# Kernel tuning notes

Measured on AMD Instinct MI355X. Metric: run time of the kernel, lower is better.

## Reference

```python
import jax, jax.numpy as jnp
import numpy as np

N = 100000      # nodes
E = 1600000     # edges
F_IN = 512      # num_node_features
HID = 128       # hidden_dim (GCN2Conv channels)
C = 64          # num_classes
L = 8           # n_layers
ALPHA = 0.1
THETA = 0.5


def setup_inputs() -> dict:
    key = jax.random.key(0)
    ks = jax.random.split(key, 7)
    x = jax.random.normal(ks[0], (N, F_IN), jnp.float32)
    edge_index = jax.random.randint(ks[1], (2, E), 0, N, dtype=jnp.int64)
    # fcs[0]: Linear(F_IN, HID); stored as [in, out] so forward is x @ w + b
    w_in = jax.random.normal(ks[2], (F_IN, HID), jnp.float32) / np.sqrt(F_IN)
    b_in = jnp.zeros((HID,), jnp.float32)
    # one shared [H, H] weight per GCN2Conv layer (shared_weights=True)
    conv_w = jax.random.normal(ks[3], (L, HID, HID), jnp.float32) / np.sqrt(HID)
    # fcs[-1]: Linear(HID, C)
    w_out = jax.random.normal(ks[4], (HID, C), jnp.float32) / np.sqrt(HID)
    b_out = jnp.zeros((C,), jnp.float32)
    return dict(x=x, edge_index=edge_index, w_in=w_in, b_in=b_in,
                conv_w=conv_w, w_out=w_out, b_out=b_out)


def _gcn_norm(edge_index, num_nodes):
    # PyG gcn_norm with add_self_loops=True, edge_weight=1
    loops = jnp.arange(num_nodes, dtype=edge_index.dtype)
    src = jnp.concatenate([edge_index[0], loops])
    dst = jnp.concatenate([edge_index[1], loops])
    deg = jax.ops.segment_sum(jnp.ones_like(dst, jnp.float32), dst,
                              num_segments=num_nodes)
    dinv = jnp.where(deg > 0, jax.lax.rsqrt(jnp.maximum(deg, 1e-12)), 0.0)
    norm = dinv[src] * dinv[dst]  # [E + N]
    return src, dst, norm


def reference(x, edge_index, w_in, b_in, conv_w, w_out, b_out):
    src, dst, norm = _gcn_norm(edge_index, N)
    h = x @ w_in + b_in          # fcs[0]; [N, HID]
    h0 = h                       # initial residual
    for l in range(L):
        beta = float(np.log(THETA / (l + 1) + 1.0))
        # sparse neighbor aggregation: out[i] = sum_e norm[e] * h[src[e]]
        agg = jax.ops.segment_sum(h[src] * norm[:, None], dst, num_segments=N)
        s = (1.0 - ALPHA) * agg + ALPHA * h0           # initial residual mix
        h = jax.nn.elu((1.0 - beta) * s + beta * (s @ conv_w[l]))  # identity mapping
        # dropout omitted (eval mode / training=False)
    logits = h @ w_out + b_out   # fcs[-1]
    return jax.nn.log_softmax(logits, axis=-1)
```

## Files before the change

### kernel.cpp

```cpp
#include <hip/hip_runtime.h>
#include <math.h>

#define N_NODES 100000
#define N_EDGES 1600000
#define F_IN    512
#define HID     128
#define NCLS    64
#define NLAYERS 8
#define NT      (N_NODES / 16)
#define NSCANB  ((N_NODES + 255) / 256)

typedef __attribute__((ext_vector_type(8))) short short8;
typedef __attribute__((ext_vector_type(4))) float float4v;

#define SWZB(b) ((b) ^ ((((b) >> 8) & 3) << 4))
#define SWZC(b) ((b) ^ ((((b) >> 8) & 7) << 4))

__device__ inline unsigned short f2bf(float f) {
    unsigned int u = __float_as_uint(f);
    unsigned int r = u + 0x7fffu + ((u >> 16) & 1u);
    return (unsigned short)(r >> 16);
}
__device__ inline float bf2f(unsigned short h) {
    return __uint_as_float(((unsigned int)h) << 16);
}
__device__ inline uint4 pack8(const unsigned short* v) {
    uint4 u;
    u.x = (unsigned)v[0] | ((unsigned)v[1] << 16);
    u.y = (unsigned)v[2] | ((unsigned)v[3] << 16);
    u.z = (unsigned)v[4] | ((unsigned)v[5] << 16);
    u.w = (unsigned)v[6] | ((unsigned)v[7] << 16);
    return u;
}
__device__ inline void bf8_fma(float* a, uint4 u, float v) {
    a[0] += v * __uint_as_float(u.x << 16);
    a[1] += v * __uint_as_float(u.x & 0xffff0000u);
    a[2] += v * __uint_as_float(u.y << 16);
    a[3] += v * __uint_as_float(u.y & 0xffff0000u);
    a[4] += v * __uint_as_float(u.z << 16);
    a[5] += v * __uint_as_float(u.z & 0xffff0000u);
    a[6] += v * __uint_as_float(u.w << 16);
    a[7] += v * __uint_as_float(u.w & 0xffff0000u);
}
__device__ inline void unpack8(float* f, uint4 u) {
    f[0] = __uint_as_float(u.x << 16); f[1] = __uint_as_float(u.x & 0xffff0000u);
    f[2] = __uint_as_float(u.y << 16); f[3] = __uint_as_float(u.y & 0xffff0000u);
    f[4] = __uint_as_float(u.z << 16); f[5] = __uint_as_float(u.z & 0xffff0000u);
    f[6] = __uint_as_float(u.w << 16); f[7] = __uint_as_float(u.w & 0xffff0000u);
}
__device__ inline void split_into(short8& ahi, short8& alo, int j, float f) {
    unsigned short h = f2bf(f);
    ahi[j] = (short)h;
    alo[j] = (short)f2bf(f - bf2f(h));
}


__global__ __launch_bounds__(256) void cnt_init(int* __restrict__ cnt) {
    int i = blockIdx.x * 256 + threadIdx.x;
    if (i < N_NODES) cnt[i] = 0;
}
__global__ __launch_bounds__(256) void cnt_count(const int* __restrict__ dst,
                                                 int* __restrict__ cnt) {
    int e = blockIdx.x * 256 + threadIdx.x;
    if (e < N_EDGES) atomicAdd(&cnt[dst[e]], 1);
}
__global__ __launch_bounds__(256) void make_dinv(const int* __restrict__ cnt,
                                                 float* __restrict__ dinv) {
    int i = blockIdx.x * 256 + threadIdx.x;
    if (i < N_NODES) dinv[i] = rsqrtf((float)(cnt[i] + 1));
}
__global__ __launch_bounds__(256) void scan_block(const int* __restrict__ cnt,
                                                  int* __restrict__ partial,
                                                  int* __restrict__ bsum) {
    __shared__ int tmp[256];
    int t = threadIdx.x, i = blockIdx.x * 256 + t;
    int v = (i < N_NODES) ? cnt[i] : 0;
    tmp[t] = v;
    __syncthreads();
#pragma unroll
    for (int off = 1; off < 256; off <<= 1) {
        int add = (t >= off) ? tmp[t - off] : 0;
        __syncthreads();
        tmp[t] += add;
        __syncthreads();
    }
    if (i < N_NODES) partial[i] = tmp[t];
    if (t == 255) bsum[blockIdx.x] = tmp[255];
}
__global__ __launch_bounds__(256) void scan_b2(int* __restrict__ b) {
    __shared__ int ps[256];
    int t = threadIdx.x;
    int i0 = 2 * t, i1 = 2 * t + 1;
    int v0 = (i0 < NSCANB) ? b[i0] : 0;
    int v1 = (i1 < NSCANB) ? b[i1] : 0;
    int s = v0 + v1;
    ps[t] = s;
    __syncthreads();
#pragma unroll
    for (int off = 1; off < 256; off <<= 1) {
        int add = (t >= off) ? ps[t - off] : 0;
        __syncthreads();
        ps[t] += add;
        __syncthreads();
    }
    int excl = ps[t] - s;
    if (i0 < NSCANB) b[i0] = excl;
    if (i1 < NSCANB) b[i1] = excl + v0;
}
__global__ __launch_bounds__(256) void finalize_rowptr(const int* __restrict__ cnt,
                                                       const int* __restrict__ partial,
                                                       const int* __restrict__ bsum,
                                                       int* __restrict__ row_ptr,
                                                       int* __restrict__ cursor) {
    int i = blockIdx.x * 256 + threadIdx.x;
    if (i < N_NODES) {
        int ex = partial[i] - cnt[i] + bsum[blockIdx.x];
        row_ptr[i] = ex;
        cursor[i]  = ex;
        if (i == N_NODES - 1) row_ptr[N_NODES] = ex + cnt[i];
    }
}
__global__ __launch_bounds__(256) void scatter_edges(const int* __restrict__ srcI,
                                                     const int* __restrict__ dstI,
                                                     const float* __restrict__ dinv,
                                                     int* __restrict__ cursor,
                                                     int2* __restrict__ rec) {
    int e = blockIdx.x * 256 + threadIdx.x;
    if (e < N_EDGES) {
        int s = srcI[e], d = dstI[e];
        int pos = atomicAdd(&cursor[d], 1);
        rec[pos] = make_int2(s, __float_as_int(dinv[s] * dinv[d]));
    }
}

__global__ __launch_bounds__(64) void conv_win(const float* __restrict__ w,
                                               unsigned short* __restrict__ wip) {
    int nt = blockIdx.x >> 4;
    int c  = blockIdx.x & 15;
    int lane = threadIdx.x;
    int n  = nt * 16 + (lane & 15);
    int kb = c * 32 + (lane >> 4) * 8;
    unsigned short hi[8], lo[8];
#pragma unroll
    for (int j = 0; j < 8; j++) {
        float v = w[(size_t)(kb + j) * HID + n];
        hi[j] = f2bf(v);
        lo[j] = f2bf(v - bf2f(hi[j]));
    }
    size_t base = ((size_t)c * 8 + nt) * 1024 + (size_t)lane * 8;
    *(uint4*)&wip[base]       = pack8(hi);
    *(uint4*)&wip[base + 512] = pack8(lo);
}

__global__ __launch_bounds__(64) void conv_wl(const float* __restrict__ cw,
                                              unsigned short* __restrict__ wlp) {
    int l  = blockIdx.x >> 5;
    int nt = (blockIdx.x >> 2) & 7;
    int c  = blockIdx.x & 3;
    int lane = threadIdx.x;
    float beta = logf(0.5f / (float)(l + 1) + 1.0f);
    int n  = nt * 16 + (lane & 15);
    int kb = c * 32 + (lane >> 4) * 8;
    const float* W = cw + (size_t)l * HID * HID;
    unsigned short hi[8], lo[8];
#pragma unroll
    for (int j = 0; j < 8; j++) {
        int k = kb + j;
        float v = beta * W[(size_t)k * HID + n] + ((k == n) ? (1.0f - beta) : 0.0f);
        hi[j] = f2bf(v);
        lo[j] = f2bf(v - bf2f(hi[j]));
    }
    size_t base = (size_t)l * 32768 + ((size_t)c * 8 + nt) * 1024 + (size_t)lane * 8;
    *(uint4*)&wlp[base]       = pack8(hi);
    *(uint4*)&wlp[base + 512] = pack8(lo);
}

__global__ __launch_bounds__(64) void conv_wout(const float* __restrict__ w,
                                                unsigned short* __restrict__ wop) {
    int nt = blockIdx.x >> 2;
    int c  = blockIdx.x & 3;
    int lane = threadIdx.x;
    int n  = nt * 16 + (lane & 15);
    int kb = c * 32 + (lane >> 4) * 8;
    unsigned short hi[8], lo[8];
#pragma unroll
    for (int j = 0; j < 8; j++) {
        float v = w[(size_t)(kb + j) * NCLS + n];
        hi[j] = f2bf(v);
        lo[j] = f2bf(v - bf2f(hi[j]));
    }
    size_t base = ((size_t)nt * 4 + c) * 1024 + (size_t)lane * 8;
    *(uint4*)&wop[base]       = pack8(hi);
    *(uint4*)&wop[base + 512] = pack8(lo);
}

__global__ __launch_bounds__(256) void in_gemm_mfma(const float* __restrict__ x,
        const unsigned short* __restrict__ wip, const float* __restrict__ bias,
        unsigned short* __restrict__ hb, unsigned short* __restrict__ h0b) {
    __shared__ unsigned short wlds[8192];
    __shared__ unsigned short tile[64][136];
    int tid = threadIdx.x;
    int wave = tid >> 6, lane = tid & 63;
    int t = blockIdx.x * 4 + wave;
    int m = lane & 15, q = lane >> 4;
    int tc = (t < NT) ? t : (NT - 1);

    const uint4* wg = (const uint4*)wip;
    uint4 pf0 = wg[tid];
    uint4 pf1 = wg[tid + 256];
    uint4 pf2 = wg[tid + 512];
    uint4 pf3 = wg[tid + 768];

    float4v acc[8];
#pragma unroll
    for (int nt = 0; nt < 8; nt++) acc[nt] = (float4v){0.f, 0.f, 0.f, 0.f};
    const float* xr = x + (size_t)(tc * 16 + m) * F_IN + q * 8;
    uint4* wl4 = (uint4*)wlds;

    for (int c = 0; c < 16; c++) {
        wl4[tid] = pf0; wl4[tid + 256] = pf1; wl4[tid + 512] = pf2; wl4[tid + 768] = pf3;
        __syncthreads();
        if (c < 15) {
            const uint4* wn = wg + (size_t)(c + 1) * 1024;
            pf0 = wn[tid]; pf1 = wn[tid + 256]; pf2 = wn[tid + 512]; pf3 = wn[tid + 768];
        }
        float4 x0 = *(const float4*)(xr + c * 32);
        float4 x1 = *(const float4*)(xr + c * 32 + 4);
        short8 ahi, alo;
        split_into(ahi, alo, 0, x0.x); split_into(ahi, alo, 1, x0.y);
        split_into(ahi, alo, 2, x0.z); split_into(ahi, alo, 3, x0.w);
        split_into(ahi, alo, 4, x1.x); split_into(ahi, alo, 5, x1.y);
        split_into(ahi, alo, 6, x1.z); split_into(ahi, alo, 7, x1.w);
#pragma unroll
        for (int nt = 0; nt < 8; nt++) {
            short8 bhi = *(short8*)&wlds[nt * 1024 + lane * 8];
            short8 blo = *(short8*)&wlds[nt * 1024 + 512 + lane * 8];
            acc[nt] = __builtin_amdgcn_mfma_f32_16x16x32_bf16(ahi, bhi, acc[nt], 0, 0, 0);
            acc[nt] = __builtin_amdgcn_mfma_f32_16x16x32_bf16(ahi, blo, acc[nt], 0, 0, 0);
            acc[nt] = __builtin_amdgcn_mfma_f32_16x16x32_bf16(alo, bhi, acc[nt], 0, 0, 0);
        }
        __syncthreads();
    }

    if (t < NT) {
#pragma unroll
        for (int nt = 0; nt < 8; nt++) {
            float bb = bias[nt * 16 + m];
#pragma unroll
            for (int r = 0; r < 4; r++)
                tile[wave * 16 + q * 4 + r][nt * 16 + m] = f2bf(acc[nt][r] + bb);
        }
    }
    __syncthreads();

    int nl = tid >> 2, part = tid & 3;
    int node = blockIdx.x * 64 + nl;
    if (node < N_NODES) {
        uint4* d1 = (uint4*)&hb [(size_t)node * HID + part * 32];
        uint4* d2 = (uint4*)&h0b[(size_t)node * HID + part * 32];
#pragma unroll
        for (int j = 0; j < 4; j++) {
            uint4 u = *(uint4*)&tile[nl][part * 32 + j * 8];
            d1[j] = u; d2[j] = u;
        }
    }
}

template <int LAST>
__global__ __launch_bounds__(256, 4) void spmm_gemm(const int* __restrict__ row_ptr,
        const int2* __restrict__ rec, const float* __restrict__ dinv,
        const unsigned short* __restrict__ hin, const unsigned short* __restrict__ h0b,
        const unsigned short* __restrict__ wlp, const unsigned short* __restrict__ wop,
        const float* __restrict__ obias, void* __restrict__ outp) {
    __shared__ __align__(16) unsigned short afr[16384];
    int tid = threadIdx.x;
    int wave = tid >> 6, lane = tid & 63;
    int qu = lane >> 4, fl = lane & 15;
    char* af = (char*)afr;

    int base = blockIdx.x * 64 + wave * 16;
#pragma unroll 1
    for (int g = 0; g < 4; ++g) {
        int node = base + g * 4 + qu;
        int nc = (node < N_NODES) ? node : (N_NODES - 1);
        int e0 = row_ptr[nc], e1 = row_ptr[nc + 1];
        float dd = dinv[nc];
        uint4 hv = *(const uint4*)(hin + (size_t)nc * HID + fl * 8);
        uint4 zv = *(const uint4*)(h0b + (size_t)nc * HID + fl * 8);
        float a[8] = {0.f, 0.f, 0.f, 0.f, 0.f, 0.f, 0.f, 0.f};
        int e = e0;
        for (; e + 7 < e1; e += 8) {
            int2 r0 = rec[e],     r1 = rec[e + 1], r2 = rec[e + 2], r3 = rec[e + 3];
            int2 r4 = rec[e + 4], r5 = rec[e + 5], r6 = rec[e + 6], r7 = rec[e + 7];
            uint4 u0 = *(const uint4*)(hin + (size_t)r0.x * HID + fl * 8);
            uint4 u1 = *(const uint4*)(hin + (size_t)r1.x * HID + fl * 8);
            uint4 u2 = *(const uint4*)(hin + (size_t)r2.x * HID + fl * 8);
            uint4 u3 = *(const uint4*)(hin + (size_t)r3.x * HID + fl * 8);
            uint4 u4 = *(const uint4*)(hin + (size_t)r4.x * HID + fl * 8);
            uint4 u5 = *(const uint4*)(hin + (size_t)r5.x * HID + fl * 8);
            uint4 u6 = *(const uint4*)(hin + (size_t)r6.x * HID + fl * 8);
            uint4 u7 = *(const uint4*)(hin + (size_t)r7.x * HID + fl * 8);
            bf8_fma(a, u0, __int_as_float(r0.y));
            bf8_fma(a, u1, __int_as_float(r1.y));
            bf8_fma(a, u2, __int_as_float(r2.y));
            bf8_fma(a, u3, __int_as_float(r3.y));
            bf8_fma(a, u4, __int_as_float(r4.y));
            bf8_fma(a, u5, __int_as_float(r5.y));
            bf8_fma(a, u6, __int_as_float(r6.y));
            bf8_fma(a, u7, __int_as_float(r7.y));
        }
        for (; e + 3 < e1; e += 4) {
            int2 r0 = rec[e], r1 = rec[e + 1], r2 = rec[e + 2], r3 = rec[e + 3];
            uint4 u0 = *(const uint4*)(hin + (size_t)r0.x * HID + fl * 8);
            uint4 u1 = *(const uint4*)(hin + (size_t)r1.x * HID + fl * 8);
            uint4 u2 = *(const uint4*)(hin + (size_t)r2.x * HID + fl * 8);
            uint4 u3 = *(const uint4*)(hin + (size_t)r3.x * HID + fl * 8);
            bf8_fma(a, u0, __int_as_float(r0.y));
            bf8_fma(a, u1, __int_as_float(r1.y));
            bf8_fma(a, u2, __int_as_float(r2.y));
            bf8_fma(a, u3, __int_as_float(r3.y));
        }
        for (; e < e1; ++e) {
            int2 r0 = rec[e];
            uint4 u0 = *(const uint4*)(hin + (size_t)r0.x * HID + fl * 8);
            bf8_fma(a, u0, __int_as_float(r0.y));
        }
        float d2 = dd * dd;
        float hvf[8], zvf[8];
        unpack8(hvf, hv);
        unpack8(zvf, zv);
        short8 ohi, olo;
#pragma unroll
        for (int j = 0; j < 8; ++j) {
            float o = 0.9f * (a[j] + d2 * hvf[j]) + 0.1f * zvf[j];
            split_into(ohi, olo, j, o);
        }
        int mrow = g * 4 + qu;
        int b0 = wave * 8192 + (fl >> 2) * 2048 + (fl & 3) * 256 + mrow * 16;
        *(short8*)(af + SWZB(b0)) = ohi;
        *(short8*)(af + SWZB(b0 + 1024)) = olo;
    }
    __syncthreads();

    float4v acc[8];
#pragma unroll
    for (int nt = 0; nt < 8; ++nt) acc[nt] = (float4v){0.f, 0.f, 0.f, 0.f};
    const short8* wp8 = (const short8*)wlp;
#pragma unroll
    for (int c = 0; c < 4; ++c) {
        int rb = wave * 8192 + c * 2048 + lane * 16;
        short8 ahi = *(const short8*)(af + SWZB(rb));
        short8 alo = *(const short8*)(af + SWZB(rb + 1024));
#pragma unroll
        for (int nt = 0; nt < 8; ++nt) {
            short8 bhi = wp8[(size_t)(c * 8 + nt) * 128 + lane];
            short8 blo = wp8[(size_t)(c * 8 + nt) * 128 + 64 + lane];
            acc[nt] = __builtin_amdgcn_mfma_f32_16x16x32_bf16(ahi, bhi, acc[nt], 0, 0, 0);
            acc[nt] = __builtin_amdgcn_mfma_f32_16x16x32_bf16(ahi, blo, acc[nt], 0, 0, 0);
            acc[nt] = __builtin_amdgcn_mfma_f32_16x16x32_bf16(alo, bhi, acc[nt], 0, 0, 0);
        }
    }

    if (LAST) {
        int t = blockIdx.x * 4 + wave;
        __syncthreads();
        char* wb = af + wave * 8192;
        if (t < NT) {
#pragma unroll
            for (int nt = 0; nt < 8; ++nt) {
#pragma unroll
                for (int r = 0; r < 4; ++r) {
                    float v = acc[nt][r];
                    v = (v > 0.f) ? v : (expf(v) - 1.0f);
                    unsigned short h = f2bf(v);
                    unsigned short l = f2bf(v - bf2f(h));
                    int b = (qu * 4 + r) * 256 + (nt * 16 + fl) * 2;
                    *(unsigned short*)(wb + SWZC(b)) = h;
                    *(unsigned short*)(wb + 4096 + SWZC(b)) = l;
                }
            }
        }
        __syncthreads();
        if (t < NT) {
            float4v oc[4];
#pragma unroll
            for (int nt = 0; nt < 4; ++nt) oc[nt] = (float4v){0.f, 0.f, 0.f, 0.f};
            const short8* wq = (const short8*)wop;
#pragma unroll
            for (int c = 0; c < 4; ++c) {
                int rb = fl * 256 + (c * 32 + qu * 8) * 2;
                short8 ahi = *(const short8*)(wb + SWZC(rb));
                short8 alo = *(const short8*)(wb + 4096 + SWZC(rb));
#pragma unroll
                for (int nt = 0; nt < 4; ++nt) {
                    short8 bhi = wq[(size_t)(nt * 4 + c) * 128 + lane];
                    short8 blo = wq[(size_t)(nt * 4 + c) * 128 + 64 + lane];
                    oc[nt] = __builtin_amdgcn_mfma_f32_16x16x32_bf16(ahi, bhi, oc[nt], 0, 0, 0);
                    oc[nt] = __builtin_amdgcn_mfma_f32_16x16x32_bf16(ahi, blo, oc[nt], 0, 0, 0);
                    oc[nt] = __builtin_amdgcn_mfma_f32_16x16x32_bf16(alo, bhi, oc[nt], 0, 0, 0);
                }
            }
            float* out = (float*)outp;
            float bn[4];
#pragma unroll
            for (int nt = 0; nt < 4; ++nt) bn[nt] = obias[nt * 16 + fl];
#pragma unroll
            for (int r = 0; r < 4; ++r) {
                float v0 = oc[0][r] + bn[0], v1 = oc[1][r] + bn[1];
                float v2 = oc[2][r] + bn[2], v3 = oc[3][r] + bn[3];
                float mx = fmaxf(fmaxf(v0, v1), fmaxf(v2, v3));
#pragma unroll
                for (int msk = 1; msk < 16; msk <<= 1) mx = fmaxf(mx, __shfl_xor(mx, msk));
                float ssum = expf(v0 - mx) + expf(v1 - mx) + expf(v2 - mx) + expf(v3 - mx);
#pragma unroll
                for (int msk = 1; msk < 16; msk <<= 1) ssum += __shfl_xor(ssum, msk);
                float lg = mx + logf(ssum);
                size_t ob = (size_t)(t * 16 + qu * 4 + r) * NCLS + fl;
                out[ob]      = v0 - lg;
                out[ob + 16] = v1 - lg;
                out[ob + 32] = v2 - lg;
                out[ob + 48] = v3 - lg;
            }
        }
    } else {
        __syncthreads();
        unsigned short (*tile)[136] = (unsigned short (*)[136])afr;
#pragma unroll
        for (int nt = 0; nt < 8; ++nt) {
#pragma unroll
            for (int r = 0; r < 4; ++r) {
                float v = acc[nt][r];
                v = (v > 0.f) ? v : (expf(v) - 1.0f);
                tile[wave * 16 + qu * 4 + r][nt * 16 + fl] = f2bf(v);
            }
        }
        __syncthreads();
        unsigned short* hout = (unsigned short*)outp;
        int nl = tid >> 2, part = tid & 3;
        int node = blockIdx.x * 64 + nl;
        if (node < N_NODES) {
            uint4* d1 = (uint4*)&hout[(size_t)node * HID + part * 32];
#pragma unroll
            for (int j = 0; j < 4; ++j) d1[j] = *(uint4*)&tile[nl][part * 32 + j * 8];
        }
    }
}


extern "C" void kernel_launch(void* const* d_in, const int* in_sizes, int n_in,
                              void* d_out, int out_size, void* d_ws, size_t ws_size,
                              hipStream_t stream) {
    const float* x      = (const float*)d_in[0];
    const int*   ei     = (const int*)  d_in[1];
    const float* w_in   = (const float*)d_in[2];
    const float* b_in   = (const float*)d_in[3];
    const float* conv_w = (const float*)d_in[4];
    const float* w_out  = (const float*)d_in[5];
    const float* b_out  = (const float*)d_in[6];
    float* out = (float*)d_out;

    const int* srcI = ei;
    const int* dstI = ei + N_EDGES;

    char* ws = (char*)d_ws;
    float* dinv    = (float*)(ws + 0x000000);
    int*   cnt     = (int*)  (ws + 0x080000);
    int*   partial = (int*)  (ws + 0x100000);
    int*   bsum    = (int*)  (ws + 0x180000);
    int*   row_ptr = (int*)  (ws + 0x190000);
    int*   cursor  = (int*)  (ws + 0x200000);
    int2*  rec     = (int2*) (ws + 0x280000);
    unsigned short* wip = (unsigned short*)(ws + 0xF00000);
    unsigned short* wlp = (unsigned short*)(ws + 0xF40000);
    unsigned short* wop = (unsigned short*)(ws + 0xFC0000);
    unsigned short* hb  = (unsigned short*)(ws + 0x1000000);
    unsigned short* h0b = hb + (size_t)N_NODES * HID;
    unsigned short* hb2 = h0b + (size_t)N_NODES * HID;

    int gN = (N_NODES + 255) / 256;
    int gE = (N_EDGES + 255) / 256;
    int gT = (NT + 3) / 4;

    cnt_init<<<gN, 256, 0, stream>>>(cnt);
    cnt_count<<<gE, 256, 0, stream>>>(dstI, cnt);
    make_dinv<<<gN, 256, 0, stream>>>(cnt, dinv);
    scan_block<<<NSCANB, 256, 0, stream>>>(cnt, partial, bsum);
    scan_b2<<<1, 256, 0, stream>>>(bsum);
    finalize_rowptr<<<NSCANB, 256, 0, stream>>>(cnt, partial, bsum, row_ptr, cursor);
    scatter_edges<<<gE, 256, 0, stream>>>(srcI, dstI, dinv, cursor, rec);

    conv_win<<<128, 64, 0, stream>>>(w_in, wip);
    conv_wl<<<256, 64, 0, stream>>>(conv_w, wlp);
    conv_wout<<<16, 64, 0, stream>>>(w_out, wop);

    in_gemm_mfma<<<gT, 256, 0, stream>>>(x, wip, b_in, hb, h0b);

    unsigned short* cur = hb;
    unsigned short* nxt = hb2;
    for (int l = 0; l < NLAYERS; l++) {
        const unsigned short* wl = wlp + (size_t)l * 32768;
        if (l < NLAYERS - 1) {
            spmm_gemm<0><<<gT, 256, 0, stream>>>(row_ptr, rec, dinv, cur, h0b, wl,
                                                 nullptr, nullptr, nxt);
            unsigned short* t = cur; cur = nxt; nxt = t;
        } else {
            spmm_gemm<1><<<gT, 256, 0, stream>>>(row_ptr, rec, dinv, cur, h0b, wl,
                                                 wop, b_out, out);
        }
    }
}
```

Measured before the change: 1.189 ms.

## Split SpMM from GEMM using feature-sliced planes for cache-resident gathers

Node features are stored as 8 feature planes of 16 channels each, and the fused SpMM+GEMM kernel is split in two. A new spmm_slice kernel aggregates one plane at a time, with block index interleaving slices, so each gather touches a 3.2MB plane that can stay in cache. It writes fp32 mixed features to an intermediate buffer, and a separate gemm_layer kernel reads them back for the MFMA transform. This trades an extra fp32 round trip through memory and an extra launch per layer for better gather locality, and it re-reads the edge records once per slice.

After: 2.140 ms. 80.0% more time.

```diff
diff --git a/kernel.cpp b/kernel.cpp
--- a/kernel.cpp
+++ b/kernel.cpp
@@ -9,6 +9,9 @@
 #define NLAYERS 8
 #define NT      (N_NODES / 16)
 #define NSCANB  ((N_NODES + 255) / 256)
+#define PLANEH  ((size_t)N_NODES * 16)
+#define PLANES  ((size_t)N_NODES * 16)
+#define GSLICE  (((N_NODES + 127) / 128) * 8)
 
 typedef __attribute__((ext_vector_type(8))) short short8;
 typedef __attribute__((ext_vector_type(4))) float float4v;
@@ -196,7 +199,7 @@
 
 __global__ __launch_bounds__(256) void in_gemm_mfma(const float* __restrict__ x,
         const unsigned short* __restrict__ wip, const float* __restrict__ bias,
-        unsigned short* __restrict__ hb, unsigned short* __restrict__ h0b) {
+        unsigned short* __restrict__ h_sm, unsigned short* __restrict__ h0_sm) {
     __shared__ unsigned short wlds[8192];
     __shared__ unsigned short tile[64][136];
     int tid = threadIdx.x;
@@ -253,23 +256,99 @@
     }
     __syncthreads();
 
-    int nl = tid >> 2, part = tid & 3;
-    int node = blockIdx.x * 64 + nl;
-    if (node < N_NODES) {
-        uint4* d1 = (uint4*)&hb [(size_t)node * HID + part * 32];
-        uint4* d2 = (uint4*)&h0b[(size_t)node * HID + part * 32];
-#pragma unroll
-        for (int j = 0; j < 4; j++) {
-            uint4 u = *(uint4*)&tile[nl][part * 32 + j * 8];
-            d1[j] = u; d2[j] = u;
-        }
-    }
+#pragma unroll
+    for (int k = 0; k < 2; k++) {
+        int c2 = tid + k * 256;
+        int plane = c2 >> 6, nl = c2 & 63;
+        int node = blockIdx.x * 64 + nl;
+        if (node < N_NODES) {
+            uint4 u0 = *(uint4*)&tile[nl][plane * 16];
+            uint4 u1 = *(uint4*)&tile[nl][plane * 16 + 8];
+            size_t off = (size_t)plane * PLANEH + (size_t)node * 16;
+            *(uint4*)&h_sm[off]      = u0; *(uint4*)&h_sm[off + 8]  = u1;
+            *(uint4*)&h0_sm[off]     = u0; *(uint4*)&h0_sm[off + 8] = u1;
+        }
+    }
+}
+
+__global__ __launch_bounds__(256) void spmm_slice(const int* __restrict__ row_ptr,
+        const int2* __restrict__ rec, const float* __restrict__ dinv,
+        const unsigned short* __restrict__ h_sm, const unsigned short* __restrict__ h0_sm,
+        float* __restrict__ s_sm) {
+    int slice = blockIdx.x & 7;
+    int tile  = blockIdx.x >> 3;
+    int node  = tile * 128 + (threadIdx.x >> 1);
+    int half  = threadIdx.x & 1;
+    if (node >= N_NODES) return;
+    const unsigned short* hp = h_sm + (size_t)slice * PLANEH;
+    int e0 = row_ptr[node], e1 = row_ptr[node + 1];
+    float dd = dinv[node];
+    uint4 hv = *(const uint4*)(hp + (size_t)node * 16 + half * 8);
+    uint4 zv = *(const uint4*)(h0_sm + (size_t)slice * PLANEH + (size_t)node * 16 + half * 8);
+    float a[8] = {0.f, 0.f, 0.f, 0.f, 0.f, 0.f, 0.f, 0.f};
+    const long long* rl = (const long long*)rec;
+    int e = e0;
+    for (; e + 7 < e1; e += 8) {
+        long long q0 = __builtin_nontemporal_load(rl + e);
+        long long q1 = __builtin_nontemporal_load(rl + e + 1);
+        long long q2 = __builtin_nontemporal_load(rl + e + 2);
+        long long q3 = __builtin_nontemporal_load(rl + e + 3);
+        long long q4 = __builtin_nontemporal_load(rl + e + 4);
+        long long q5 = __builtin_nontemporal_load(rl + e + 5);
+        long long q6 = __builtin_nontemporal_load(rl + e + 6);
+        long long q7 = __builtin_nontemporal_load(rl + e + 7);
+        uint4 u0 = *(const uint4*)(hp + (size_t)(int)q0 * 16 + half * 8);
+        uint4 u1 = *(const uint4*)(hp + (size_t)(int)q1 * 16 + half * 8);
+        uint4 u2 = *(const uint4*)(hp + (size_t)(int)q2 * 16 + half * 8);
+        uint4 u3 = *(const uint4*)(hp + (size_t)(int)q3 * 16 + half * 8);
+        uint4 u4 = *(const uint4*)(hp + (size_t)(int)q4 * 16 + half * 8);
+        uint4 u5 = *(const uint4*)(hp + (size_t)(int)q5 * 16 + half * 8);
+        uint4 u6 = *(const uint4*)(hp + (size_t)(int)q6 * 16 + half * 8);
+        uint4 u7 = *(const uint4*)(hp + (size_t)(int)q7 * 16 + half * 8);
+        bf8_fma(a, u0, __int_as_float((int)(q0 >> 32)));
+        bf8_fma(a, u1, __int_as_float((int)(q1 >> 32)));
+        bf8_fma(a, u2, __int_as_float((int)(q2 >> 32)));
+        bf8_fma(a, u3, __int_as_float((int)(q3 >> 32)));
+        bf8_fma(a, u4, __int_as_float((int)(q4 >> 32)));
+        bf8_fma(a, u5, __int_as_float((int)(q5 >> 32)));
+        bf8_fma(a, u6, __int_as_float((int)(q6 >> 32)));
+        bf8_fma(a, u7, __int_as_float((int)(q7 >> 32)));
+    }
+    for (; e + 3 < e1; e += 4) {
+        long long q0 = __builtin_nontemporal_load(rl + e);
+        long long q1 = __builtin_nontemporal_load(rl + e + 1);
+        long long q2 = __builtin_nontemporal_load(rl + e + 2);
+        long long q3 = __builtin_nontemporal_load(rl + e + 3);
+        uint4 u0 = *(const uint4*)(hp + (size_t)(int)q0 * 16 + half * 8);
+        uint4 u1 = *(const uint4*)(hp + (size_t)(int)q1 * 16 + half * 8);
+        uint4 u2 = *(const uint4*)(hp + (size_t)(int)q2 * 16 + half * 8);
+        uint4 u3 = *(const uint4*)(hp + (size_t)(int)q3 * 16 + half * 8);
+        bf8_fma(a, u0, __int_as_float((int)(q0 >> 32)));
+        bf8_fma(a, u1, __int_as_float((int)(q1 >> 32)));
+        bf8_fma(a, u2, __int_as_float((int)(q2 >> 32)));
+        bf8_fma(a, u3, __int_as_float((int)(q3 >> 32)));
+    }
+    for (; e < e1; ++e) {
+        long long q0 = __builtin_nontemporal_load(rl + e);
+        uint4 u0 = *(const uint4*)(hp + (size_t)(int)q0 * 16 + half * 8);
+        bf8_fma(a, u0, __int_as_float((int)(q0 >> 32)));
+    }
+    float d2 = dd * dd;
+    float hvf[8], zvf[8];
+    unpack8(hvf, hv);
+    unpack8(zvf, zv);
+    float4v s0, s1;
+#pragma unroll
+    for (int j = 0; j < 4; ++j) s0[j] = 0.9f * (a[j] + d2 * hvf[j]) + 0.1f * zvf[j];
+#pragma unroll
+    for (int j = 0; j < 4; ++j) s1[j] = 0.9f * (a[j + 4] + d2 * hvf[j + 4]) + 0.1f * zvf[j + 4];
+    float* sp = s_sm + (size_t)slice * PLANES + (size_t)node * 16 + half * 8;
+    __builtin_nontemporal_store(s0, (float4v*)sp);
+    __builtin_nontemporal_store(s1, (float4v*)(sp + 4));
 }
 
 template <int LAST>
-__global__ __launch_bounds__(256, 4) void spmm_gemm(const int* __restrict__ row_ptr,
-        const int2* __restrict__ rec, const float* __restrict__ dinv,
-        const unsigned short* __restrict__ hin, const unsigned short* __restrict__ h0b,
+__global__ __launch_bounds__(256, 4) void gemm_layer(const float* __restrict__ s_sm,
         const unsigned short* __restrict__ wlp, const unsigned short* __restrict__ wop,
         const float* __restrict__ obias, void* __restrict__ outp) {
     __shared__ __align__(16) unsigned short afr[16384];
@@ -279,66 +358,22 @@
     char* af = (char*)afr;
 
     int base = blockIdx.x * 64 + wave * 16;
-#pragma unroll 1
+#pragma unroll
     for (int g = 0; g < 4; ++g) {
         int node = base + g * 4 + qu;
         int nc = (node < N_NODES) ? node : (N_NODES - 1);
-        int e0 = row_ptr[nc], e1 = row_ptr[nc + 1];
-        float dd = dinv[nc];
-        uint4 hv = *(const uint4*)(hin + (size_t)nc * HID + fl * 8);
-        uint4 zv = *(const uint4*)(h0b + (size_t)nc * HID + fl * 8);
-        float a[8] = {0.f, 0.f, 0.f, 0.f, 0.f, 0.f, 0.f, 0.f};
-        int e = e0;
-        for (; e + 7 < e1; e += 8) {
-            int2 r0 = rec[e],     r1 = rec[e + 1], r2 = rec[e + 2], r3 = rec[e + 3];
-            int2 r4 = rec[e + 4], r5 = rec[e + 5], r6 = rec[e + 6], r7 = rec[e + 7];
-            uint4 u0 = *(const uint4*)(hin + (size_t)r0.x * HID + fl * 8);
-            uint4 u1 = *(const uint4*)(hin + (size_t)r1.x * HID + fl * 8);
-            uint4 u2 = *(const uint4*)(hin + (size_t)r2.x * HID + fl * 8);
-            uint4 u3 = *(const uint4*)(hin + (size_t)r3.x * HID + fl * 8);
-            uint4 u4 = *(const uint4*)(hin + (size_t)r4.x * HID + fl * 8);
-            uint4 u5 = *(const uint4*)(hin + (size_t)r5.x * HID + fl * 8);
-            uint4 u6 = *(const uint4*)(hin + (size_t)r6.x * HID + fl * 8);
-            uint4 u7 = *(const uint4*)(hin + (size_t)r7.x * HID + fl * 8);
-            bf8_fma(a, u0, __int_as_float(r0.y));
-            bf8_fma(a, u1, __int_as_float(r1.y));
-            bf8_fma(a, u2, __int_as_float(r2.y));
-            bf8_fma(a, u3, __int_as_float(r3.y));
-            bf8_fma(a, u4, __int_as_float(r4.y));
-            bf8_fma(a, u5, __int_as_float(r5.y));
-            bf8_fma(a, u6, __int_as_float(r6.y));
-            bf8_fma(a, u7, __int_as_float(r7.y));
-        }
-        for (; e + 3 < e1; e += 4) {
-            int2 r0 = rec[e], r1 = rec[e + 1], r2 = rec[e + 2], r3 = rec[e + 3];
-            uint4 u0 = *(const uint4*)(hin + (size_t)r0.x * HID + fl * 8);
-            uint4 u1 = *(const uint4*)(hin + (size_t)r1.x * HID + fl * 8);
-            uint4 u2 = *(const uint4*)(hin + (size_t)r2.x * HID + fl * 8);
-            uint4 u3 = *(const uint4*)(hin + (size_t)r3.x * HID + fl * 8);
-            bf8_fma(a, u0, __int_as_float(r0.y));
-            bf8_fma(a, u1, __int_as_float(r1.y));
-            bf8_fma(a, u2, __int_as_float(r2.y));
-            bf8_fma(a, u3, __int_as_float(r3.y));
-        }
-        for (; e < e1; ++e) {
-            int2 r0 = rec[e];
-            uint4 u0 = *(const uint4*)(hin + (size_t)r0.x * HID + fl * 8);
-            bf8_fma(a, u0, __int_as_float(r0.y));
-        }
-        float d2 = dd * dd;
-        float hvf[8], zvf[8];
-        unpack8(hvf, hv);
-        unpack8(zvf, zv);
-        short8 ohi, olo;
-#pragma unroll
-        for (int j = 0; j < 8; ++j) {
-            float o = 0.9f * (a[j] + d2 * hvf[j]) + 0.1f * zvf[j];
-            split_into(ohi, olo, j, o);
-        }
+        const float* sp = s_sm + (size_t)(fl >> 1) * PLANES + (size_t)nc * 16 + (fl & 1) * 8;
+        float4v x0 = __builtin_nontemporal_load((const float4v*)sp);
+        float4v x1 = __builtin_nontemporal_load((const float4v*)(sp + 4));
+        short8 ahi, alo;
+        split_into(ahi, alo, 0, x0[0]); split_into(ahi, alo, 1, x0[1]);
+        split_into(ahi, alo, 2, x0[2]); split_into(ahi, alo, 3, x0[3]);
+        split_into(ahi, alo, 4, x1[0]); split_into(ahi, alo, 5, x1[1]);
+        split_into(ahi, alo, 6, x1[2]); split_into(ahi, alo, 7, x1[3]);
         int mrow = g * 4 + qu;
         int b0 = wave * 8192 + (fl >> 2) * 2048 + (fl & 3) * 256 + mrow * 16;
-        *(short8*)(af + SWZB(b0)) = ohi;
-        *(short8*)(af + SWZB(b0 + 1024)) = olo;
+        *(short8*)(af + SWZB(b0)) = ahi;
+        *(short8*)(af + SWZB(b0 + 1024)) = alo;
     }
     __syncthreads();
 
@@ -436,12 +471,18 @@
         }
         __syncthreads();
         unsigned short* hout = (unsigned short*)outp;
-        int nl = tid >> 2, part = tid & 3;
-        int node = blockIdx.x * 64 + nl;
-        if (node < N_NODES) {
-            uint4* d1 = (uint4*)&hout[(size_t)node * HID + part * 32];
-#pragma unroll
-            for (int j = 0; j < 4; ++j) d1[j] = *(uint4*)&tile[nl][part * 32 + j * 8];
+#pragma unroll
+        for (int k = 0; k < 2; k++) {
+            int c2 = tid + k * 256;
+            int plane = c2 >> 6, nl = c2 & 63;
+            int node = blockIdx.x * 64 + nl;
+            if (node < N_NODES) {
+                uint4 u0 = *(uint4*)&tile[nl][plane * 16];
+                uint4 u1 = *(uint4*)&tile[nl][plane * 16 + 8];
+                size_t off = (size_t)plane * PLANEH + (size_t)node * 16;
+                *(uint4*)&hout[off]     = u0;
+                *(uint4*)&hout[off + 8] = u1;
+            }
         }
     }
 }
@@ -473,9 +514,10 @@
     unsigned short* wip = (unsigned short*)(ws + 0xF00000);
     unsigned short* wlp = (unsigned short*)(ws + 0xF40000);
     unsigned short* wop = (unsigned short*)(ws + 0xFC0000);
-    unsigned short* hb  = (unsigned short*)(ws + 0x1000000);
-    unsigned short* h0b = hb + (size_t)N_NODES * HID;
-    unsigned short* hb2 = h0b + (size_t)N_NODES * HID;
+    unsigned short* h1  = (unsigned short*)(ws + 0x1000000);
+    unsigned short* h0s = h1 + 8 * PLANEH;
+    unsigned short* h2  = h0s + 8 * PLANEH;
+    float* s_sm = (float*)(h2 + 8 * PLANEH);
 
     int gN = (N_NODES + 255) / 256;
     int gE = (N_EDGES + 255) / 256;
@@ -493,19 +535,18 @@
     conv_wl<<<256, 64, 0, stream>>>(conv_w, wlp);
     conv_wout<<<16, 64, 0, stream>>>(w_out, wop);
 
-    in_gemm_mfma<<<gT, 256, 0, stream>>>(x, wip, b_in, hb, h0b);
-
-    unsigned short* cur = hb;
-    unsigned short* nxt = hb2;
+    in_gemm_mfma<<<gT, 256, 0, stream>>>(x, wip, b_in, h1, h0s);
+
+    unsigned short* cur = h1;
+    unsigned short* nxt = h2;
     for (int l = 0; l < NLAYERS; l++) {
         const unsigned short* wl = wlp + (size_t)l * 32768;
+        spmm_slice<<<GSLICE, 256, 0, stream>>>(row_ptr, rec, dinv, cur, h0s, s_sm);
         if (l < NLAYERS - 1) {
-            spmm_gemm<0><<<gT, 256, 0, stream>>>(row_ptr, rec, dinv, cur, h0b, wl,
-                                                 nullptr, nullptr, nxt);
+            gemm_layer<0><<<gT, 256, 0, stream>>>(s_sm, wl, nullptr, nullptr, nxt);
             unsigned short* t = cur; cur = nxt; nxt = t;
         } else {
-            spmm_gemm<1><<<gT, 256, 0, stream>>>(row_ptr, rec, dinv, cur, h0b, wl,
-                                                 wop, b_out, out);
-        }
-    }
-}
+            gemm_layer<1><<<gT, 256, 0, stream>>>(s_sm, wl, wop, b_out, out);
+        }
+    }
+}
```
